# Optimization experiments

Measured on AMD Instinct MI355X. Metric: run time of the kernel, lower is better.

## Reference

```python
import jax, jax.numpy as jnp
import numpy as np

N = 100000      # nodes
E = 600000      # directed edges (before self-loops)
NFEAT = 128
NHID = 128
NCLASS = 64


def setup_inputs() -> dict:
    key = jax.random.key(0)
    k1, k2, k3, k4 = jax.random.split(key, 4)
    x = jax.random.normal(k1, (N, NFEAT), dtype=jnp.float32)
    edge_index = jax.random.randint(k2, (2, E), 0, N, dtype=jnp.int32)
    # GCNConv learned params (Glorot-ish init), bias zeros as in PyG default
    W1 = jax.random.normal(k3, (NFEAT, NHID), dtype=jnp.float32) / jnp.sqrt(NFEAT)
    b1 = jnp.zeros((NHID,), dtype=jnp.float32)
    W2 = jax.random.normal(k4, (NHID, NCLASS), dtype=jnp.float32) / jnp.sqrt(NHID)
    b2 = jnp.zeros((NCLASS,), dtype=jnp.float32)
    return {"x": x, "edge_index": edge_index, "W1": W1, "b1": b1, "W2": W2, "b2": b2}


def _gcn_layer(x, src, dst, norm, W, b, n):
    # PyG GCNConv: linear transform, then normalized neighbor aggregation, then bias
    h = x @ W                                   # [N, out]
    msg = h[src] * norm[:, None]                # [E+N, out] gather + scale
    agg = jax.ops.segment_sum(msg, dst, num_segments=n)  # scatter-add
    return agg + b


def reference(x, edge_index, W1, b1, W2, b2):
    n = x.shape[0]
    # add self-loops (PyG gcn_norm default add_self_loops=True)
    loops = jnp.arange(n, dtype=edge_index.dtype)
    src = jnp.concatenate([edge_index[0], loops])
    dst = jnp.concatenate([edge_index[1], loops])
    # symmetric normalization: D^-1/2 (A+I) D^-1/2
    deg = jax.ops.segment_sum(jnp.ones_like(dst, dtype=x.dtype), dst, num_segments=n)
    d_inv_sqrt = jnp.where(deg > 0, jax.lax.rsqrt(deg), 0.0)
    norm = d_inv_sqrt[src] * d_inv_sqrt[dst]
    h = jax.nn.relu(_gcn_layer(x, src, dst, norm, W1, b1, n))
    # F.dropout with training=False is identity -> omitted in eval reference
    return _gcn_layer(h, src, dst, norm, W2, b2, n)
```

## Files before the change

kernel.cpp:

```cpp
#include <hip/hip_runtime.h>


typedef unsigned short u16;
typedef unsigned int u32;
typedef __attribute__((ext_vector_type(8))) short bf16x8;
typedef __attribute__((ext_vector_type(4))) float f32x4;

__device__ __forceinline__ float b2f(u16 s) {
  return __uint_as_float(((u32)s) << 16);
}
__device__ __forceinline__ u16 f2b(float f) {
  u32 u = __float_as_uint(f);
  u32 r = (u + 0x7FFFu + ((u >> 16) & 1u)) >> 16;
  return (u16)r;
}
__device__ __forceinline__ u32 pk2(float a, float b) {
  return (u32)f2b(a) | ((u32)f2b(b) << 16);
}
__device__ __forceinline__ void dec8(uint4 v, float f[8]) {
  f[0] = __uint_as_float(v.x << 16);
  f[1] = __uint_as_float(v.x & 0xFFFF0000u);
  f[2] = __uint_as_float(v.y << 16);
  f[3] = __uint_as_float(v.y & 0xFFFF0000u);
  f[4] = __uint_as_float(v.z << 16);
  f[5] = __uint_as_float(v.z & 0xFFFF0000u);
  f[6] = __uint_as_float(v.w << 16);
  f[7] = __uint_as_float(v.w & 0xFFFF0000u);
}
__device__ __forceinline__ void fma8(uint4 v, float d, float acc[8]) {
  acc[0] = fmaf(__uint_as_float(v.x << 16), d, acc[0]);
  acc[1] = fmaf(__uint_as_float(v.x & 0xFFFF0000u), d, acc[1]);
  acc[2] = fmaf(__uint_as_float(v.y << 16), d, acc[2]);
  acc[3] = fmaf(__uint_as_float(v.y & 0xFFFF0000u), d, acc[3]);
  acc[4] = fmaf(__uint_as_float(v.z << 16), d, acc[4]);
  acc[5] = fmaf(__uint_as_float(v.z & 0xFFFF0000u), d, acc[5]);
  acc[6] = fmaf(__uint_as_float(v.w << 16), d, acc[6]);
  acc[7] = fmaf(__uint_as_float(v.w & 0xFFFF0000u), d, acc[7]);
}


__global__ __launch_bounds__(256) void prep_k(const void* __restrict__ W1,
                                              const void* __restrict__ b1,
                                              const void* __restrict__ W2,
                                              const void* __restrict__ b2,
                                              u16* __restrict__ W1b, u16* __restrict__ ob1,
                                              u16* __restrict__ W2t, u16* __restrict__ ob2,
                                              int* __restrict__ mode,
                                              int* __restrict__ cnt, int np) {
  __shared__ int cnt_s;
  const int tid = threadIdx.x;
  int i = blockIdx.x * 256 + tid;
  if (i < np) cnt[i] = 0;

  if (tid == 0) cnt_s = 0;
  __syncthreads();
  int c = 0;
  for (int j = tid; j < 4096; j += 256) {
    u32 e = (((const u16*)W1)[j] >> 7) & 0xFFu;
    if (e >= 100u && e <= 130u) c++;
  }
  atomicAdd(&cnt_s, c);
  __syncthreads();
  const int m = (cnt_s < 3328) ? 1 : 0;
  if (blockIdx.x == 0 && tid == 0) *mode = m;

  if (i < 24768) {
    int j = i;
    const void* src;
    u16* dst;
    int sidx, didx;
    if (j < 16384) {
      src = W1; dst = W1b; sidx = j; didx = j;
    } else if ((j -= 16384) < 128) {
      src = b1; dst = ob1; sidx = j; didx = j;
    } else if ((j -= 128) < 8192) {
      int nn = j >> 7, k = j & 127;
      src = W2; dst = W2t; sidx = k * 64 + nn; didx = j;
    } else {
      j -= 8192;
      src = b2; dst = ob2; sidx = j; didx = j;
    }
    dst[didx] = m ? f2b(((const float*)src)[sidx]) : ((const u16*)src)[sidx];
  }
}


__global__ __launch_bounds__(256) void count_k(const int* __restrict__ dst,
                                               int* __restrict__ cnt, int E) {
  int e = blockIdx.x * 256 + threadIdx.x;
  if (e < E) atomicAdd(&cnt[dst[e]], 1);
}

__global__ __launch_bounds__(256) void scan1(const int* __restrict__ cnt,
                                             int* __restrict__ offs,
                                             int* __restrict__ bsum, int np) {
  __shared__ int lds[256];
  int t = threadIdx.x;
  int i = blockIdx.x * 256 + t;
  int v = cnt[i];
  lds[t] = v;
  __syncthreads();
#pragma unroll
  for (int off = 1; off < 256; off <<= 1) {
    int add = (t >= off) ? lds[t - off] : 0;
    __syncthreads();
    lds[t] += add;
    __syncthreads();
  }
  offs[i] = lds[t] - v;
  if (t == 0) bsum[blockIdx.x] = lds[255];
}

__global__ __launch_bounds__(256) void scan23(const int* __restrict__ offs,
                                              const int* __restrict__ bsum,
                                              int* __restrict__ cursor,
                                              const int* __restrict__ cnt,
                                              float* __restrict__ dinv,
                                              int4* __restrict__ ninfo, int np) {
  __shared__ int lds[256];
  const int t = threadIdx.x, b = blockIdx.x;
  int part = 0;
  for (int k = t; k < b; k += 256) part += bsum[k];
  lds[t] = part;
  __syncthreads();
#pragma unroll
  for (int off = 128; off > 0; off >>= 1) {
    if (t < off) lds[t] += lds[t + off];
    __syncthreads();
  }
  const int pre = lds[0];
  int i = b * 256 + t;
  int o = offs[i] + pre;
  cursor[i] = o;
  int c = cnt[i];
  float dv = rsqrtf((float)c + 1.0f);
  dinv[i] = dv;
  ninfo[i] = make_int4(o, c, __float_as_int(dv), 0);
}

__global__ __launch_bounds__(256) void fill_k(const int* __restrict__ src,
                                              const int* __restrict__ dst,
                                              int* __restrict__ cursor,
                                              const float* __restrict__ dinv,
                                              int2* __restrict__ sp, int E) {
  int e = blockIdx.x * 256 + threadIdx.x;
  if (e < E) {
    int s = src[e];
    float ds = dinv[s];
    int p = atomicAdd(&cursor[dst[e]], 1);
    sp[p] = make_int2(s, __float_as_int(ds));
  }
}


__global__ __launch_bounds__(256) void gemm1_k(const void* __restrict__ Araw,
                                               const u16* __restrict__ W,
                                               u16* __restrict__ out, int M,
                                               const int* __restrict__ mode) {
  __shared__ __align__(16) u16 Wt[128 * 136];
  __shared__ __align__(16) u16 As[64 * 136];
  const int tid = threadIdx.x;
  const int mcv = *mode;

  for (int idx = tid; idx < 128 * 128; idx += 256) {
    int n = idx & 127;
    int k = idx >> 7;
    Wt[n * 136 + k] = W[k * 128 + n];
  }
  __syncthreads();

  const int wv = tid >> 6, lane = tid & 63, lr = lane & 15, lq = lane >> 4;
  const int ntiles = (M + 63) >> 6;

  for (int t = blockIdx.x; t < ntiles; t += gridDim.x) {
    const int r0 = t * 64;
    __syncthreads();
    for (int idx = tid; idx < 64 * 16; idx += 256) {
      int row = idx >> 4, c = idx & 15;
      uint4 v = make_uint4(0u, 0u, 0u, 0u);
      if (r0 + row < M) {
        if (mcv) {
          const float* xf = (const float*)Araw + (size_t)(r0 + row) * 128 + c * 8;
          float4 f0 = *(const float4*)xf;
          float4 f1 = *(const float4*)(xf + 4);
          v.x = pk2(f0.x, f0.y);
          v.y = pk2(f0.z, f0.w);
          v.z = pk2(f1.x, f1.y);
          v.w = pk2(f1.z, f1.w);
        } else {
          v = *(const uint4*)((const u16*)Araw + (size_t)(r0 + row) * 128 + c * 8);
        }
      }
      *(uint4*)&As[row * 136 + c * 8] = v;
    }
    __syncthreads();

    bf16x8 a[4];
#pragma unroll
    for (int s = 0; s < 4; ++s)
      a[s] = *(const bf16x8*)&As[(wv * 16 + lr) * 136 + s * 32 + lq * 8];

#pragma unroll
    for (int nt = 0; nt < 8; ++nt) {
      f32x4 acc = {0.f, 0.f, 0.f, 0.f};
#pragma unroll
      for (int s = 0; s < 4; ++s) {
        bf16x8 b = *(const bf16x8*)&Wt[(nt * 16 + lr) * 136 + s * 32 + lq * 8];
        acc = __builtin_amdgcn_mfma_f32_16x16x32_bf16(a[s], b, acc, 0, 0, 0);
      }
#pragma unroll
      for (int r = 0; r < 4; ++r) {
        int row = r0 + wv * 16 + lq * 4 + r;
        if (row < M) out[(size_t)row * 128 + nt * 16 + lr] = f2b(acc[r]);
      }
    }
  }
}


__global__ __launch_bounds__(256) void fusedB_k(const u16* __restrict__ h,
                                                const int2* __restrict__ sp,
                                                const int4* __restrict__ ninfo,
                                                const u16* __restrict__ b1,
                                                const u16* __restrict__ W2t,
                                                u16* __restrict__ g, int n) {
  __shared__ __align__(16) u16 As[16 * 136];
  const int tid = threadIdx.x, wv = tid >> 6, lane = tid & 63;
  const int lq = lane >> 4, lr = lane & 15;
  const int base = blockIdx.x * 16;
  const int i = base + wv * 4 + lq;
  const bool valid = (i < n);

  int start = 0, c = 0;
  float di = 0.f;
  if (valid) {
    int4 ni = ninfo[i];
    start = ni.x;
    c = ni.y;
    di = __int_as_float(ni.z);
  }
  float acc[8];
  {
    uint4 v = valid ? *(const uint4*)(h + (size_t)i * 128 + lr * 8)
                    : make_uint4(0u, 0u, 0u, 0u);
    float f[8];
    dec8(v, f);
#pragma unroll
    for (int j = 0; j < 8; ++j) acc[j] = f[j] * di;
  }
  const int bl = lq * 16;
  for (int bs = 0; __any(bs < c); bs += 16) {
    int m = c - bs;
    m = m < 0 ? 0 : (m > 16 ? 16 : m);
    int s = 0, db = 0;
    if (lr < m) {
      int2 p = sp[start + bs + lr];
      s = p.x;
      db = p.y;
    }
    int mmw = m;
    mmw = max(mmw, __shfl_xor(mmw, 16));
    mmw = max(mmw, __shfl_xor(mmw, 32));
    for (int e = 0; e < mmw; e += 4) {
      int s0 = __shfl(s, bl + e), s1 = __shfl(s, bl + e + 1);
      int s2 = __shfl(s, bl + e + 2), s3 = __shfl(s, bl + e + 3);
      float d0 = __int_as_float(__shfl(db, bl + e));
      float d1 = __int_as_float(__shfl(db, bl + e + 1));
      float d2 = __int_as_float(__shfl(db, bl + e + 2));
      float d3 = __int_as_float(__shfl(db, bl + e + 3));
      uint4 v0 = *(const uint4*)(h + (size_t)s0 * 128 + lr * 8);
      uint4 v1 = *(const uint4*)(h + (size_t)s1 * 128 + lr * 8);
      uint4 v2 = *(const uint4*)(h + (size_t)s2 * 128 + lr * 8);
      uint4 v3 = *(const uint4*)(h + (size_t)s3 * 128 + lr * 8);
      fma8(v0, d0, acc);
      fma8(v1, d1, acc);
      fma8(v2, d2, acc);
      fma8(v3, d3, acc);
    }
  }
  {
    uint4 bv = *(const uint4*)(b1 + lr * 8);
    float bf[8];
    dec8(bv, bf);
    float o[8];
#pragma unroll
    for (int j = 0; j < 8; ++j) o[j] = fmaxf(fmaf(acc[j], di, bf[j]), 0.f);
    uint4 ov;
    ov.x = pk2(o[0], o[1]);
    ov.y = pk2(o[2], o[3]);
    ov.z = pk2(o[4], o[5]);
    ov.w = pk2(o[6], o[7]);
    *(uint4*)&As[(wv * 4 + lq) * 136 + lr * 8] = ov;
  }
  __syncthreads();

  bf16x8 a[4];
#pragma unroll
  for (int s = 0; s < 4; ++s)
    a[s] = *(const bf16x8*)&As[lr * 136 + s * 32 + lq * 8];
  {
    const int nt = wv;
    f32x4 acc4 = {0.f, 0.f, 0.f, 0.f};
#pragma unroll
    for (int s = 0; s < 4; ++s) {
      bf16x8 b = *(const bf16x8*)&W2t[(nt * 16 + lr) * 128 + s * 32 + lq * 8];
      acc4 = __builtin_amdgcn_mfma_f32_16x16x32_bf16(a[s], b, acc4, 0, 0, 0);
    }
#pragma unroll
    for (int r = 0; r < 4; ++r) {
      int row = base + lq * 4 + r;
      if (row < n) g[(size_t)row * 64 + nt * 16 + lr] = f2b(acc4[r]);
    }
  }
}


__global__ __launch_bounds__(256) void agg2_k(const u16* __restrict__ g,
                                              const int2* __restrict__ sp,
                                              const int4* __restrict__ ninfo,
                                              const u16* __restrict__ b2,
                                              void* __restrict__ outv, int n,
                                              const int* __restrict__ mode) {
  const int lane = threadIdx.x & 63;
  const int o8 = lane >> 3, l8 = lane & 7;
  const int i = blockIdx.x * 32 + (threadIdx.x >> 6) * 8 + o8;
  const bool valid = (i < n);

  int start = 0, c = 0;
  float di = 0.f;
  if (valid) {
    int4 ni = ninfo[i];
    start = ni.x;
    c = ni.y;
    di = __int_as_float(ni.z);
  }
  float acc[8];
  {
    uint4 v = valid ? *(const uint4*)(g + (size_t)i * 64 + l8 * 8)
                    : make_uint4(0u, 0u, 0u, 0u);
    float f[8];
    dec8(v, f);
#pragma unroll
    for (int j = 0; j < 8; ++j) acc[j] = f[j] * di;
  }
  const int bl = o8 * 8;
  for (int base = 0; __any(base < c); base += 8) {
    int m = c - base;
    m = m < 0 ? 0 : (m > 8 ? 8 : m);
    int s = 0, db = 0;
    if (l8 < m) {
      int2 p = sp[start + base + l8];
      s = p.x;
      db = p.y;
    }
    int mmw = m;
    mmw = max(mmw, __shfl_xor(mmw, 8));
    mmw = max(mmw, __shfl_xor(mmw, 16));
    mmw = max(mmw, __shfl_xor(mmw, 32));
    for (int e = 0; e < mmw; e += 4) {
      int s0 = __shfl(s, bl + e), s1 = __shfl(s, bl + e + 1);
      int s2 = __shfl(s, bl + e + 2), s3 = __shfl(s, bl + e + 3);
      float d0 = __int_as_float(__shfl(db, bl + e));
      float d1 = __int_as_float(__shfl(db, bl + e + 1));
      float d2 = __int_as_float(__shfl(db, bl + e + 2));
      float d3 = __int_as_float(__shfl(db, bl + e + 3));
      uint4 v0 = *(const uint4*)(g + (size_t)s0 * 64 + l8 * 8);
      uint4 v1 = *(const uint4*)(g + (size_t)s1 * 64 + l8 * 8);
      uint4 v2 = *(const uint4*)(g + (size_t)s2 * 64 + l8 * 8);
      uint4 v3 = *(const uint4*)(g + (size_t)s3 * 64 + l8 * 8);
      fma8(v0, d0, acc);
      fma8(v1, d1, acc);
      fma8(v2, d2, acc);
      fma8(v3, d3, acc);
    }
  }
  if (valid) {
    uint4 bv = *(const uint4*)(b2 + l8 * 8);
    float bf[8];
    dec8(bv, bf);
    float o[8];
#pragma unroll
    for (int j = 0; j < 8; ++j) o[j] = fmaf(acc[j], di, bf[j]);
    if (*mode) {
      float* op = (float*)outv + (size_t)i * 64 + l8 * 8;
      *(float4*)op = make_float4(o[0], o[1], o[2], o[3]);
      *(float4*)(op + 4) = make_float4(o[4], o[5], o[6], o[7]);
    } else {
      uint4 ov;
      ov.x = pk2(o[0], o[1]);
      ov.y = pk2(o[2], o[3]);
      ov.z = pk2(o[4], o[5]);
      ov.w = pk2(o[6], o[7]);
      *(uint4*)((u16*)outv + (size_t)i * 64 + l8 * 8) = ov;
    }
  }
}


extern "C" void kernel_launch(void* const* d_in, const int* in_sizes, int n_in,
                              void* d_out, int out_size, void* d_ws, size_t ws_size,
                              hipStream_t stream) {
  const void* x_raw  = d_in[0];
  const int*  ei     = (const int*)d_in[1];
  const void* W1_raw = d_in[2];
  const void* b1_raw = d_in[3];
  const void* W2_raw = d_in[4];
  const void* b2_raw = d_in[5];

  const int N = in_sizes[0] / 128;
  const int E = in_sizes[1] / 2;
  const int NP = ((N + 255) / 256) * 256;
  const int NB = NP / 256;

  char* ws = (char*)d_ws;
  size_t off = 0;
  auto alloc = [&](size_t bytes) -> void* {
    void* p = ws + off;
    off = (off + bytes + 255) & ~(size_t)255;
    return p;
  };
  int*   mode   = (int*)alloc(4);
  int*   cnt    = (int*)alloc((size_t)NP * 4);
  float* dinv   = (float*)alloc((size_t)NP * 4);
  int*   offs   = (int*)alloc((size_t)NP * 4);
  int*   cursor = (int*)alloc((size_t)NP * 4);
  int*   bsum   = (int*)alloc(1024 * 4);
  int4*  ninfo  = (int4*)alloc((size_t)NP * 16);
  int2*  sp     = (int2*)alloc((size_t)E * 8);
  u16*   W1b    = (u16*)alloc((size_t)128 * 128 * 2);
  u16*   b1b    = (u16*)alloc(128 * 2);
  u16*   W2t    = (u16*)alloc((size_t)64 * 128 * 2);
  u16*   b2b    = (u16*)alloc(64 * 2);
  u16*   h      = (u16*)alloc((size_t)N * 128 * 2);
  u16*   g      = (u16*)alloc((size_t)N * 64 * 2);

  const int eb = (E + 255) / 256;
  prep_k<<<NB, 256, 0, stream>>>(W1_raw, b1_raw, W2_raw, b2_raw,
                                 W1b, b1b, W2t, b2b, mode, cnt, NP);
  count_k<<<eb, 256, 0, stream>>>(ei + E, cnt, E);
  scan1<<<NB, 256, 0, stream>>>(cnt, offs, bsum, NP);
  scan23<<<NB, 256, 0, stream>>>(offs, bsum, cursor, cnt, dinv, ninfo, NP);
  fill_k<<<eb, 256, 0, stream>>>(ei, ei + E, cursor, dinv, sp, E);
  gemm1_k<<<512, 256, 0, stream>>>(x_raw, W1b, h, N, mode);
  fusedB_k<<<(N + 15) / 16, 256, 0, stream>>>(h, sp, ninfo, b1b, W2t, g, N);
  agg2_k<<<(N + 31) / 32, 256, 0, stream>>>(g, sp, ninfo, b2b, d_out, N, mode);
}
```

Measured before the change: 241.9 us.

## Merge prep with degree count and fill with GEMM into shared launches

Folds the degree-count atomics into the weight-prep kernel as extra blocks, and replaces the memset of counts with hipMemsetAsync. Runs the CSR fill and the first GEMM in one launch using disjoint block ranges, so the two independent jobs overlap. Fill blocks are split into 8 destination-range groups, each scanning a 1/32 slice of the edges, so atomics on a given cursor range stay local. The cost is that every edge is read 8 times by fill blocks, and the fill blocks reserve the GEMM's LDS without using it, which may limit occupancy.

```diff
diff --git a/kernel.cpp b/kernel.cpp
--- a/kernel.cpp
+++ b/kernel.cpp
@@ -39,18 +39,23 @@
 }
 
 
-__global__ __launch_bounds__(256) void prep_k(const void* __restrict__ W1,
-                                              const void* __restrict__ b1,
-                                              const void* __restrict__ W2,
-                                              const void* __restrict__ b2,
-                                              u16* __restrict__ W1b, u16* __restrict__ ob1,
-                                              u16* __restrict__ W2t, u16* __restrict__ ob2,
-                                              int* __restrict__ mode,
-                                              int* __restrict__ cnt, int np) {
+__global__ __launch_bounds__(256) void prepcount_k(const void* __restrict__ W1,
+                                                   const void* __restrict__ b1,
+                                                   const void* __restrict__ W2,
+                                                   const void* __restrict__ b2,
+                                                   u16* __restrict__ W1b, u16* __restrict__ ob1,
+                                                   u16* __restrict__ W2t, u16* __restrict__ ob2,
+                                                   int* __restrict__ mode,
+                                                   const int* __restrict__ dst,
+                                                   int* __restrict__ cnt, int E, int NB) {
   __shared__ int cnt_s;
   const int tid = threadIdx.x;
-  int i = blockIdx.x * 256 + tid;
-  if (i < np) cnt[i] = 0;
+
+  if ((int)blockIdx.x >= NB) {
+    int e = ((int)blockIdx.x - NB) * 256 + tid;
+    if (e < E) atomicAdd(&cnt[dst[e]], 1);
+    return;
+  }
 
   if (tid == 0) cnt_s = 0;
   __syncthreads();
@@ -64,32 +69,27 @@
   const int m = (cnt_s < 3328) ? 1 : 0;
   if (blockIdx.x == 0 && tid == 0) *mode = m;
 
+  int i = blockIdx.x * 256 + tid;
   if (i < 24768) {
     int j = i;
     const void* src;
-    u16* dst;
+    u16* dstp;
     int sidx, didx;
     if (j < 16384) {
-      src = W1; dst = W1b; sidx = j; didx = j;
+      src = W1; dstp = W1b; sidx = j; didx = j;
     } else if ((j -= 16384) < 128) {
-      src = b1; dst = ob1; sidx = j; didx = j;
+      src = b1; dstp = ob1; sidx = j; didx = j;
     } else if ((j -= 128) < 8192) {
       int nn = j >> 7, k = j & 127;
-      src = W2; dst = W2t; sidx = k * 64 + nn; didx = j;
+      src = W2; dstp = W2t; sidx = k * 64 + nn; didx = j;
     } else {
       j -= 8192;
-      src = b2; dst = ob2; sidx = j; didx = j;
-    }
-    dst[didx] = m ? f2b(((const float*)src)[sidx]) : ((const u16*)src)[sidx];
-  }
-}
-
-
-__global__ __launch_bounds__(256) void count_k(const int* __restrict__ dst,
-                                               int* __restrict__ cnt, int E) {
-  int e = blockIdx.x * 256 + threadIdx.x;
-  if (e < E) atomicAdd(&cnt[dst[e]], 1);
-}
+      src = b2; dstp = ob2; sidx = j; didx = j;
+    }
+    dstp[didx] = m ? f2b(((const float*)src)[sidx]) : ((const u16*)src)[sidx];
+  }
+}
+
 
 __global__ __launch_bounds__(256) void scan1(const int* __restrict__ cnt,
                                              int* __restrict__ offs,
@@ -138,41 +138,56 @@
   ninfo[i] = make_int4(o, c, __float_as_int(dv), 0);
 }
 
-__global__ __launch_bounds__(256) void fill_k(const int* __restrict__ src,
-                                              const int* __restrict__ dst,
-                                              int* __restrict__ cursor,
-                                              const float* __restrict__ dinv,
-                                              int2* __restrict__ sp, int E) {
-  int e = blockIdx.x * 256 + threadIdx.x;
-  if (e < E) {
-    int s = src[e];
-    float ds = dinv[s];
-    int p = atomicAdd(&cursor[dst[e]], 1);
-    sp[p] = make_int2(s, __float_as_int(ds));
-  }
-}
-
-
-__global__ __launch_bounds__(256) void gemm1_k(const void* __restrict__ Araw,
-                                               const u16* __restrict__ W,
-                                               u16* __restrict__ out, int M,
-                                               const int* __restrict__ mode) {
+
+#define FILLB 256
+#define GEMMB 512
+
+__global__ __launch_bounds__(256) void fillgemm_k(const int* __restrict__ srcA,
+                                                  const int* __restrict__ dstA,
+                                                  int* __restrict__ cursor,
+                                                  const float* __restrict__ dinv,
+                                                  int2* __restrict__ sp, int E, int n,
+                                                  const void* __restrict__ Araw,
+                                                  const u16* __restrict__ W,
+                                                  u16* __restrict__ out, int M,
+                                                  const int* __restrict__ mode) {
   __shared__ __align__(16) u16 Wt[128 * 136];
   __shared__ __align__(16) u16 As[64 * 136];
   const int tid = threadIdx.x;
+
+  if ((int)blockIdx.x < FILLB) {
+    const int g = blockIdx.x & 7;
+    const int j = blockIdx.x >> 3;
+    const int NPG = (n + 7) >> 3;
+    const int lo = g * NPG;
+    const int hi = min(n, lo + NPG);
+    const int chunk = (E + 31) >> 5;
+    const int e1 = min(E, (j + 1) * chunk);
+    for (int e = j * chunk + tid; e < e1; e += 256) {
+      int d = dstA[e];
+      int s = srcA[e];
+      if (d >= lo && d < hi) {
+        float ds = dinv[s];
+        int p = atomicAdd(&cursor[d], 1);
+        sp[p] = make_int2(s, __float_as_int(ds));
+      }
+    }
+    return;
+  }
+
   const int mcv = *mode;
 
   for (int idx = tid; idx < 128 * 128; idx += 256) {
-    int n = idx & 127;
+    int nn = idx & 127;
     int k = idx >> 7;
-    Wt[n * 136 + k] = W[k * 128 + n];
+    Wt[nn * 136 + k] = W[k * 128 + nn];
   }
   __syncthreads();
 
   const int wv = tid >> 6, lane = tid & 63, lr = lane & 15, lq = lane >> 4;
   const int ntiles = (M + 63) >> 6;
 
-  for (int t = blockIdx.x; t < ntiles; t += gridDim.x) {
+  for (int t = (int)blockIdx.x - FILLB; t < ntiles; t += GEMMB) {
     const int r0 = t * 64;
     __syncthreads();
     for (int idx = tid; idx < 64 * 16; idx += 256) {
@@ -435,13 +450,15 @@
   u16*   g      = (u16*)alloc((size_t)N * 64 * 2);
 
   const int eb = (E + 255) / 256;
-  prep_k<<<NB, 256, 0, stream>>>(W1_raw, b1_raw, W2_raw, b2_raw,
-                                 W1b, b1b, W2t, b2b, mode, cnt, NP);
-  count_k<<<eb, 256, 0, stream>>>(ei + E, cnt, E);
+
+  hipMemsetAsync(cnt, 0, (size_t)NP * 4, stream);
+  prepcount_k<<<NB + eb, 256, 0, stream>>>(W1_raw, b1_raw, W2_raw, b2_raw,
+                                           W1b, b1b, W2t, b2b, mode,
+                                           ei + E, cnt, E, NB);
   scan1<<<NB, 256, 0, stream>>>(cnt, offs, bsum, NP);
   scan23<<<NB, 256, 0, stream>>>(offs, bsum, cursor, cnt, dinv, ninfo, NP);
-  fill_k<<<eb, 256, 0, stream>>>(ei, ei + E, cursor, dinv, sp, E);
-  gemm1_k<<<512, 256, 0, stream>>>(x_raw, W1b, h, N, mode);
+  fillgemm_k<<<FILLB + GEMMB, 256, 0, stream>>>(ei, ei + E, cursor, dinv, sp, E, N,
+                                                x_raw, W1b, h, N, mode);
   fusedB_k<<<(N + 15) / 16, 256, 0, stream>>>(h, sp, ninfo, b1b, W2t, g, N);
   agg2_k<<<(N + 31) / 32, 256, 0, stream>>>(g, sp, ninfo, b2b, d_out, N, mode);
 }
```

New measurement: 265.8 us. 1.1x slower.
